# Kernel optimization log

Hardware: AMD Instinct MI355X
Metric: run time of the kernel (lower is better)

## Reference

```python
import jax, jax.numpy as jnp
import numpy as np

DIM = 1024
NUM_HEADS = 8
HEAD_DIM = 64
QK_DIM = NUM_HEADS * HEAD_DIM  # 512
B, S = 4, 1024


def setup_inputs() -> dict:
    key = jax.random.key(0)
    k1, k2, k3, k4, k5 = jax.random.split(key, 5)
    x = jax.random.normal(k1, (B, S, DIM), dtype=jnp.float32)
    mask = jax.random.randint(k2, (B, S), 0, 2).astype(bool)
    rotator = jax.random.normal(k3, (B, S, HEAD_DIM, HEAD_DIM), dtype=jnp.float32)
    # Linear weights stored as [in, out] for x @ W
    w_t = jax.random.normal(k4, (DIM, 2 * QK_DIM + DIM), dtype=jnp.float32) * (DIM ** -0.5)
    w_o = jax.random.normal(k5, (DIM, DIM), dtype=jnp.float32) * (DIM ** -0.5)
    return {"x": x, "mask": mask, "rotator": rotator, "w_t": w_t, "w_o": w_o}


def taylor_atn_fn(qs, ks, vs, mask):
    # 2nd-order Taylor approximation of softmax attention:
    # exp(s) ~= 1 + s + s^2/2, with invalid keys masked out.
    scale = HEAD_DIM ** -0.5
    s = jnp.einsum('bqhd,bkhd->bhqk', qs, ks) * scale  # [B,H,S,S]
    scores = 1.0 + s + 0.5 * s * s
    scores = scores * mask[:, None, None, :].astype(scores.dtype)  # mask keys
    denom = jnp.maximum(jnp.sum(scores, axis=-1), 1e-6)            # [B,H,Q]
    out = jnp.einsum('bhqk,bkhd->bqhd', scores, vs)
    out = out / jnp.transpose(denom, (0, 2, 1))[..., None]         # [B,Q,H,vd]
    return out.reshape(out.shape[0], out.shape[1], -1)


def reference(x, mask, rotator, w_t, w_o):
    t = x @ w_t                                   # [B,S,2*QK+DIM]
    Bx, Sx = t.shape[0], t.shape[1]
    qs = t[..., :QK_DIM].reshape(Bx, Sx, NUM_HEADS, HEAD_DIM)
    ks = t[..., QK_DIM:2 * QK_DIM].reshape(Bx, Sx, NUM_HEADS, HEAD_DIM)
    vs = t[..., 2 * QK_DIM:].reshape(Bx, Sx, NUM_HEADS, -1)
    m = mask[..., None, None]
    # masked per-position rotation: q -> R q, k -> R^T k
    qs = jnp.where(m, jnp.einsum('bsij,bshj->bshi', rotator, qs), qs)
    ks = jnp.where(m, jnp.einsum('bsij,bshi->bshj', rotator, ks), ks)
    out = taylor_atn_fn(qs, ks, vs, mask)
    return out @ w_o
```

## Files before the change

kernel.cpp:

```cpp
#include <hip/hip_runtime.h>
#include <cstdint>
#include <cstddef>

#define DIMX  1024
#define NH    8
#define HD    64
#define QKD   512
#define VDD   128
#define BATCH 4
#define SEQ   1024
#define NPOS  (BATCH*SEQ)
#define TW    (2*QKD + DIMX)
#define SCALE 0.125f

typedef __bf16 bf16x8 __attribute__((ext_vector_type(8)));
typedef float  f32x4  __attribute__((ext_vector_type(4)));
typedef float  f32x16 __attribute__((ext_vector_type(16)));

__device__ __forceinline__ ushort f2bf(float f) {
    unsigned b = __float_as_uint(f);
    return (ushort)((b + 0x7FFFu + ((b >> 16) & 1u)) >> 16);
}

__device__ __forceinline__ unsigned cvtpk(float lo, float hi) {
    unsigned r;
    asm("v_cvt_pk_bf16_f32 %0, %1, %2" : "=v"(r) : "v"(lo), "v"(hi));
    return r;
}

__device__ __forceinline__ void plswap(unsigned &a, unsigned &b) {
    asm("v_permlane32_swap_b32 %0, %1" : "+v"(a), "+v"(b));
}

#define GLD16(src, dst) __builtin_amdgcn_global_load_lds(                      \
    (const __attribute__((address_space(1))) unsigned int*)(src),              \
    (__attribute__((address_space(3))) unsigned int*)(dst), 16, 0, 0)

#define SW(row, col) ((row)*64 + ((col) ^ (((row)&7)<<3)))

__device__ __forceinline__ int2 xcd_swz(int gx, int gy) {
    const int nwg = gx * gy;
    int id = blockIdx.y * gx + blockIdx.x;
    id = (id & 7) * (nwg >> 3) + (id >> 3);
    return make_int2(id % gx, id / gx);
}

__global__ __launch_bounds__(256)
void cast_bf16(const float* __restrict__ in, ushort* __restrict__ out, int n4)
{
    const int i = blockIdx.x * 256 + threadIdx.x;
    if (i >= n4) return;
    float4 v = *(const float4*)(in + (size_t)i * 4);
    ushort4 o;
    o.x = f2bf(v.x); o.y = f2bf(v.y); o.z = f2bf(v.z); o.w = f2bf(v.w);
    *(ushort4*)(out + (size_t)i * 4) = o;
}

__global__ __launch_bounds__(256)
void transpose_cast(const float* __restrict__ W, ushort* __restrict__ WT,
                    int K, int N)
{
    __shared__ float tile[32][33];
    const int bn = blockIdx.x * 32;
    const int bk = blockIdx.y * 32;
    const int tx = threadIdx.x & 31;
    const int ty = threadIdx.x >> 5;
    #pragma unroll
    for (int i = ty; i < 32; i += 8)
        tile[i][tx] = W[(size_t)(bk + i) * N + bn + tx];
    __syncthreads();
    #pragma unroll
    for (int i = ty; i < 32; i += 8)
        WT[(size_t)(bn + i) * K + bk + tx] = f2bf(tile[tx][i]);
}

__global__ __launch_bounds__(256, 2)
void gemm_qkv(const ushort* __restrict__ A, const ushort* __restrict__ BT,
              float* __restrict__ t1, ushort* __restrict__ Vt)
{
    const int K = DIMX, N = TW;
    __shared__ __align__(16) ushort lA[128 * 32];
    __shared__ __align__(16) ushort lB[128 * 32];

    const int2 bij = xcd_swz(N/128, NPOS/128);
    const int tid  = threadIdx.x;
    const int lane = tid & 63;
    const int wave = tid >> 6;
    const int wr   = wave >> 1;
    const int wc   = wave & 1;
    const int bm   = bij.y * 128;
    const int bn   = bij.x * 128;

    const int r0 = wave * 32 + (lane >> 2);
    const int kc = (lane & 3) * 8;
    const ushort* a0 = A  + (size_t)(bm + r0) * K + kc;
    const ushort* a1 = A  + (size_t)(bm + r0 + 16) * K + kc;
    const ushort* b0 = BT + (size_t)(bn + r0) * K + kc;
    const ushort* b1 = BT + (size_t)(bn + r0 + 16) * K + kc;
    ushort* lA0 = lA + wave * 1024;
    ushort* lA1 = lA0 + 512;
    ushort* lB0 = lB + wave * 1024;
    ushort* lB1 = lB0 + 512;

    const int fr = lane & 15;
    const int kh = (lane >> 4) * 8;
    const ushort* ra = lA + (wr * 64 + fr) * 32 + kh;
    const ushort* rb = lB + (wc * 64 + fr) * 32 + kh;

    f32x4 acc[4][4] = {};

    for (int k0 = 0; k0 < K; k0 += 32) {
        GLD16(a0 + k0, lA0);
        GLD16(a1 + k0, lA1);
        GLD16(b0 + k0, lB0);
        GLD16(b1 + k0, lB1);
        asm volatile("s_waitcnt vmcnt(0)" ::: "memory");
        __syncthreads();
        bf16x8 af[4], bfr[4];
        #pragma unroll
        for (int m = 0; m < 4; ++m) af[m]  = *(const bf16x8*)(ra + m * 512);
        #pragma unroll
        for (int n = 0; n < 4; ++n) bfr[n] = *(const bf16x8*)(rb + n * 512);
        #pragma unroll
        for (int m = 0; m < 4; ++m)
            #pragma unroll
            for (int n = 0; n < 4; ++n)
                acc[m][n] = __builtin_amdgcn_mfma_f32_16x16x32_bf16(
                    af[m], bfr[n], acc[m][n], 0, 0, 0);
        __syncthreads();
    }

    const int orow = (lane >> 4) * 4;
    if (bn < 1024) {
        #pragma unroll
        for (int m = 0; m < 4; ++m)
            #pragma unroll
            for (int n = 0; n < 4; ++n) {
                float* dst = t1 + (size_t)(bm + wr * 64 + m * 16 + orow) * 1024
                               + bn + wc * 64 + n * 16 + fr;
                #pragma unroll
                for (int q = 0; q < 4; ++q)
                    dst[(size_t)q * 1024] = acc[m][n][q];
            }
    } else {
        #pragma unroll
        for (int m = 0; m < 4; ++m)
            #pragma unroll
            for (int n = 0; n < 4; ++n) {
                const int row0 = bm + wr * 64 + m * 16 + orow;
                const int cv   = bn + wc * 64 + n * 16 + fr - 1024;
                const int hh = cv >> 7, vd = cv & 127;
                const int bb = row0 >> 10, ss = row0 & 1023;
                ushort o4[4];
                #pragma unroll
                for (int q = 0; q < 4; ++q) o4[q] = f2bf(acc[m][n][q]);
                *(ushort4*)&Vt[((size_t)(bb*NH + hh)*VDD + vd)*SEQ + ss] =
                    *(ushort4*)o4;
            }
    }
}

__global__ __launch_bounds__(256, 2)
void gemm_bf16_mfma(const ushort* __restrict__ A, const ushort* __restrict__ BT,
                    float* __restrict__ C, int M, int N, int K)
{
    __shared__ __align__(16) ushort lA[128 * 32];
    __shared__ __align__(16) ushort lB[128 * 32];

    const int2 bij = xcd_swz(N/128, M/128);
    const int tid  = threadIdx.x;
    const int lane = tid & 63;
    const int wave = tid >> 6;
    const int wr   = wave >> 1;
    const int wc   = wave & 1;
    const int bm   = bij.y * 128;
    const int bn   = bij.x * 128;

    const int r0 = wave * 32 + (lane >> 2);
    const int kc = (lane & 3) * 8;
    const ushort* a0 = A  + (size_t)(bm + r0) * K + kc;
    const ushort* a1 = A  + (size_t)(bm + r0 + 16) * K + kc;
    const ushort* b0 = BT + (size_t)(bn + r0) * K + kc;
    const ushort* b1 = BT + (size_t)(bn + r0 + 16) * K + kc;
    ushort* lA0 = lA + wave * 1024;
    ushort* lA1 = lA0 + 512;
    ushort* lB0 = lB + wave * 1024;
    ushort* lB1 = lB0 + 512;

    const int fr = lane & 15;
    const int kh = (lane >> 4) * 8;
    const ushort* ra = lA + (wr * 64 + fr) * 32 + kh;
    const ushort* rb = lB + (wc * 64 + fr) * 32 + kh;

    f32x4 acc[4][4] = {};

    for (int k0 = 0; k0 < K; k0 += 32) {
        GLD16(a0 + k0, lA0);
        GLD16(a1 + k0, lA1);
        GLD16(b0 + k0, lB0);
        GLD16(b1 + k0, lB1);
        asm volatile("s_waitcnt vmcnt(0)" ::: "memory");
        __syncthreads();
        bf16x8 af[4], bfr[4];
        #pragma unroll
        for (int m = 0; m < 4; ++m) af[m]  = *(const bf16x8*)(ra + m * 512);
        #pragma unroll
        for (int n = 0; n < 4; ++n) bfr[n] = *(const bf16x8*)(rb + n * 512);
        #pragma unroll
        for (int m = 0; m < 4; ++m)
            #pragma unroll
            for (int n = 0; n < 4; ++n)
                acc[m][n] = __builtin_amdgcn_mfma_f32_16x16x32_bf16(
                    af[m], bfr[n], acc[m][n], 0, 0, 0);
        __syncthreads();
    }

    const int orow = (lane >> 4) * 4;
    #pragma unroll
    for (int m = 0; m < 4; ++m)
        #pragma unroll
        for (int n = 0; n < 4; ++n) {
            float* dst = C + (size_t)(bm + wr * 64 + m * 16 + orow) * N
                           + bn + wc * 64 + n * 16 + fr;
            #pragma unroll
            for (int q = 0; q < 4; ++q)
                dst[(size_t)q * N] = acc[m][n][q];
        }
}

__global__ __launch_bounds__(256)
void rotate_pack_qk(const float* __restrict__ t1, const int* __restrict__ mask,
                    const float* __restrict__ rot, ushort* __restrict__ Qb,
                    ushort* __restrict__ Kb)
{
    const int p   = blockIdx.x;
    const int tid = threadIdx.x;
    const int b = p >> 10, s = p & 1023;
    const bool rotated = (mask[p] != 0);

    __shared__ float R[64][69];
    __shared__ float qv[QKD];
    __shared__ float kv[QKD];

    const float* tq = t1 + (size_t)p * 1024;
    {
        float2 q2 = *(const float2*)(tq + tid*2);
        float2 k2 = *(const float2*)(tq + QKD + tid*2);
        qv[tid*2]   = q2.x; qv[tid*2+1] = q2.y;
        kv[tid*2]   = k2.x; kv[tid*2+1] = k2.y;
        if (rotated) {
            const float* Rg = rot + (size_t)p * 4096;
            const int base = tid * 16;
            const int r = base >> 6, c = base & 63;
            #pragma unroll
            for (int x = 0; x < 16; x += 4) {
                float4 v = *(const float4*)(Rg + base + x);
                R[r][c+x+0] = v.x; R[r][c+x+1] = v.y;
                R[r][c+x+2] = v.z; R[r][c+x+3] = v.w;
            }
        }
    }
    __syncthreads();

    #pragma unroll
    for (int ph = 0; ph < 2; ++ph) {
        const int h = (tid >> 6) + ph*4;
        const int i = tid & 63;
        const float* qh  = &qv[h*64];
        const float* kh2 = &kv[h*64];
        float aq, ak;
        if (rotated) {
            aq = 0.f; ak = 0.f;
            #pragma unroll 8
            for (int j = 0; j < 64; ++j) {
                aq = fmaf(R[i][j], qh[j], aq);
                ak = fmaf(R[j][i], kh2[j], ak);
            }
        } else {
            aq = qh[i]; ak = kh2[i];
        }
        const size_t dst = ((size_t)(b*NH + h)*SEQ + s)*HD + i;
        Qb[dst] = f2bf(aq * SCALE);
        Kb[dst] = f2bf(ak);
    }
}

__global__ __launch_bounds__(256, 2)
void taylor_attn_mfma(const ushort* __restrict__ Qb, const ushort* __restrict__ Kb,
                      const ushort* __restrict__ Vt, const int* __restrict__ mask,
                      ushort* __restrict__ attn)
{
    const int bh  = blockIdx.x;
    const int qt  = blockIdx.y;
    const int b   = bh >> 3, h = bh & 7;
    const int tid = threadIdx.x;
    const int lane = tid & 63;
    const int wave = tid >> 6;
    const int kh  = wave >> 1;
    const int qg  = wave & 1;
    const int l31 = lane & 31;
    const int g   = lane >> 5;

    __shared__ __align__(16) ushort smem[32768];
    __shared__ float mskAll[SEQ];
    __shared__ float dpart[64];
    __shared__ float dinv2[64];

    ushort* Ksp = smem + kh * 8192;
    ushort* Vsp = smem + 16384 + kh * 8192;
    float*  comb = (float*)smem;

    {
        int4 mv = *(const int4*)(mask + b*SEQ + tid*4);
        float4 f = make_float4(mv.x ? 1.f : 0.f, mv.y ? 1.f : 0.f,
                               mv.z ? 1.f : 0.f, mv.w ? 1.f : 0.f);
        *(float4*)&mskAll[tid*4] = f;
    }

    const ushort* qrow = Qb + ((size_t)bh*SEQ + qt*64 + qg*32 + l31) * HD + g*8;
    bf16x8 qf[4];
    #pragma unroll
    for (int ds = 0; ds < 4; ++ds) qf[ds] = *(const bf16x8*)(qrow + ds*16);

    const int sub  = lane >> 3;
    const int scol = ((lane & 7) * 8) ^ (sub << 3);
    const ushort* Kbase = Kb + (size_t)bh*SEQ*HD;
    const ushort* Vbase = Vt + (size_t)bh*VDD*SEQ;

#define ISSUE_K(buf, ktn) do {                                                 \
    _Pragma("unroll")                                                          \
    for (int i_ = 0; i_ < 4; ++i_)                                             \
        GLD16(Kbase + ((size_t)(ktn)*64 + 8*(qg*4+i_) + sub)*HD + scol,        \
              Ksp + (buf)*4096 + (qg*4+i_)*512);                               \
} while (0)
#define ISSUE_V(ktn) do {                                                      \
    _Pragma("unroll")                                                          \
    for (int i_ = 0; i_ < 8; ++i_)                                             \
        GLD16(Vbase + (size_t)(8*(qg*8+i_) + sub)*SEQ + (ktn)*64 + scol,       \
              Vsp + (qg*8+i_)*512);                                            \
} while (0)

    f32x16 acc[4] = {};
    float dacc = 0.f;

    ISSUE_K(0, kh*8);
    asm volatile("s_waitcnt vmcnt(0)" ::: "memory");
    __syncthreads();

    for (int it = 0; it < 8; ++it) {
        const int kt = kh*8 + it;
        const int cb = it & 1;
        ISSUE_V(kt);
        if (it < 7) ISSUE_K(cb ^ 1, kt + 1);

        f32x16 sf0 = {}, sf1 = {};
        __builtin_amdgcn_s_setprio(1);
        #pragma unroll
        for (int ds = 0; ds < 4; ++ds) {
            const int dc = ds*16 + g*8;
            bf16x8 kf0 = *(const bf16x8*)&Ksp[cb*4096 + SW(l31, dc)];
            bf16x8 kf1 = *(const bf16x8*)&Ksp[cb*4096 + SW(32 + l31, dc)];
            sf0 = __builtin_amdgcn_mfma_f32_32x32x16_bf16(kf0, qf[ds], sf0, 0, 0, 0);
            sf1 = __builtin_amdgcn_mfma_f32_32x32x16_bf16(kf1, qf[ds], sf1, 0, 0, 0);
        }
        __builtin_amdgcn_s_setprio(0);

        const float* mrow = mskAll + kt*64;
        unsigned w0[8], w1[8];
        float dadd = 0.f;
        #pragma unroll
        for (int rr = 0; rr < 4; ++rr) {
            const float4 mqa = *(const float4*)&mrow[8*rr + 4*g];
            const float4 mqb = *(const float4*)&mrow[32 + 8*rr + 4*g];
            float s0 = sf0[rr*4+0], s1 = sf0[rr*4+1];
            float s2 = sf0[rr*4+2], s3 = sf0[rr*4+3];
            float c0 = fmaf(fmaf(0.5f*s0, s0, s0), mqa.x, mqa.x);
            float c1 = fmaf(fmaf(0.5f*s1, s1, s1), mqa.y, mqa.y);
            float c2 = fmaf(fmaf(0.5f*s2, s2, s2), mqa.z, mqa.z);
            float c3 = fmaf(fmaf(0.5f*s3, s3, s3), mqa.w, mqa.w);
            float t0 = sf1[rr*4+0], t1 = sf1[rr*4+1];
            float t2 = sf1[rr*4+2], t3 = sf1[rr*4+3];
            float d0 = fmaf(fmaf(0.5f*t0, t0, t0), mqb.x, mqb.x);
            float d1 = fmaf(fmaf(0.5f*t1, t1, t1), mqb.y, mqb.y);
            float d2 = fmaf(fmaf(0.5f*t2, t2, t2), mqb.z, mqb.z);
            float d3 = fmaf(fmaf(0.5f*t3, t3, t3), mqb.w, mqb.w);
            dadd += ((c0+c1)+(c2+c3)) + ((d0+d1)+(d2+d3));
            w0[rr*2+0] = cvtpk(c0, c1);
            w0[rr*2+1] = cvtpk(c2, c3);
            w1[rr*2+0] = cvtpk(d0, d1);
            w1[rr*2+1] = cvtpk(d2, d3);
        }
        dacc += dadd;
        plswap(w0[0], w0[2]); plswap(w0[1], w0[3]);
        plswap(w0[4], w0[6]); plswap(w0[5], w0[7]);
        plswap(w1[0], w1[2]); plswap(w1[1], w1[3]);
        plswap(w1[4], w1[6]); plswap(w1[5], w1[7]);

        asm volatile("s_waitcnt vmcnt(0)" ::: "memory");
        __syncthreads();

        __builtin_amdgcn_s_setprio(1);
        #pragma unroll
        for (int kq = 0; kq < 4; ++kq) {
            union { unsigned u[4]; bf16x8 v; } pu;
            if (kq == 0)      { pu.u[0]=w0[0]; pu.u[1]=w0[1]; pu.u[2]=w0[2]; pu.u[3]=w0[3]; }
            else if (kq == 1) { pu.u[0]=w0[4]; pu.u[1]=w0[5]; pu.u[2]=w0[6]; pu.u[3]=w0[7]; }
            else if (kq == 2) { pu.u[0]=w1[0]; pu.u[1]=w1[1]; pu.u[2]=w1[2]; pu.u[3]=w1[3]; }
            else              { pu.u[0]=w1[4]; pu.u[1]=w1[5]; pu.u[2]=w1[6]; pu.u[3]=w1[7]; }
            const int kcol = kq*16 + g*8;
            acc[0] = __builtin_amdgcn_mfma_f32_32x32x16_bf16(
                pu.v, *(const bf16x8*)&Vsp[SW(      l31, kcol)], acc[0], 0, 0, 0);
            acc[1] = __builtin_amdgcn_mfma_f32_32x32x16_bf16(
                pu.v, *(const bf16x8*)&Vsp[SW( 32 + l31, kcol)], acc[1], 0, 0, 0);
            acc[2] = __builtin_amdgcn_mfma_f32_32x32x16_bf16(
                pu.v, *(const bf16x8*)&Vsp[SW( 64 + l31, kcol)], acc[2], 0, 0, 0);
            acc[3] = __builtin_amdgcn_mfma_f32_32x32x16_bf16(
                pu.v, *(const bf16x8*)&Vsp[SW( 96 + l31, kcol)], acc[3], 0, 0, 0);
        }
        __builtin_amdgcn_s_setprio(0);
        __syncthreads();
    }
#undef ISSUE_K
#undef ISSUE_V

    const float dhalf = dacc + __shfl_xor(dacc, 32);

    if (kh == 1) {
        float* cbp = comb + qg * 4096;
        #pragma unroll
        for (int vb = 0; vb < 4; ++vb)
            #pragma unroll
            for (int rr = 0; rr < 4; ++rr) {
                float4 v = make_float4(acc[vb][rr*4+0], acc[vb][rr*4+1],
                                       acc[vb][rr*4+2], acc[vb][rr*4+3]);
                *(float4*)&cbp[(vb*32 + l31)*32 + 4*g + 8*rr] = v;
            }
        if (lane < 32) dpart[qg*32 + l31] = dhalf;
    }
    __syncthreads();
    if (kh == 0) {
        float* cbp = comb + qg * 4096;
        const float dtot = dhalf + dpart[qg*32 + l31];
        if (lane < 32) dinv2[qg*32 + l31] = 1.f / fmaxf(dtot, 1e-6f);
        #pragma unroll
        for (int vb = 0; vb < 4; ++vb)
            #pragma unroll
            for (int rr = 0; rr < 4; ++rr) {
                float4 v = *(const float4*)&cbp[(vb*32 + l31)*32 + 4*g + 8*rr];
                acc[vb][rr*4+0] += v.x; acc[vb][rr*4+1] += v.y;
                acc[vb][rr*4+2] += v.z; acc[vb][rr*4+3] += v.w;
            }
        float inv[16];
        #pragma unroll
        for (int rr = 0; rr < 4; ++rr) {
            float4 iv = *(const float4*)&dinv2[qg*32 + 8*rr + 4*g];
            inv[rr*4+0] = iv.x; inv[rr*4+1] = iv.y;
            inv[rr*4+2] = iv.z; inv[rr*4+3] = iv.w;
        }
        ushort* obase = attn + ((size_t)(b*SEQ + qt*64 + qg*32)) * DIMX
                      + h*VDD + l31;
        #pragma unroll
        for (int vb = 0; vb < 4; ++vb)
            #pragma unroll
            for (int rr = 0; rr < 4; ++rr)
                #pragma unroll
                for (int j = 0; j < 4; ++j) {
                    const int q = 4*g + 8*rr + j;
                    obase[(size_t)q*DIMX + vb*32] = f2bf(acc[vb][rr*4+j] * inv[rr*4+j]);
                }
    }
}

extern "C" void kernel_launch(void* const* d_in, const int* in_sizes, int n_in,
                              void* d_out, int out_size, void* d_ws, size_t ws_size,
                              hipStream_t stream)
{
    const float* x    = (const float*)d_in[0];
    const int*   mask = (const int*)d_in[1];
    const float* rot  = (const float*)d_in[2];
    const float* w_t  = (const float*)d_in[3];
    const float* w_o  = (const float*)d_in[4];
    float* out = (float*)d_out;

    float*  t1     = (float*)d_ws;
    ushort* xbf    = (ushort*)(t1 + (size_t)NPOS * 1024);
    ushort* attnbf = xbf;
    ushort* wtT    = xbf + (size_t)NPOS * DIMX;
    ushort* woT    = wtT + (size_t)TW * DIMX;
    ushort* Qb     = woT + (size_t)DIMX * DIMX;
    ushort* Kb     = Qb  + (size_t)BATCH * NH * SEQ * HD;
    ushort* Vtp    = Kb  + (size_t)BATCH * NH * SEQ * HD;

    cast_bf16<<<(NPOS*DIMX/4 + 255)/256, 256, 0, stream>>>(x, xbf, NPOS*DIMX/4);
    transpose_cast<<<dim3(TW/32, DIMX/32),   256, 0, stream>>>(w_t, wtT, DIMX, TW);
    transpose_cast<<<dim3(DIMX/32, DIMX/32), 256, 0, stream>>>(w_o, woT, DIMX, DIMX);

    gemm_qkv<<<dim3(TW/128, NPOS/128), 256, 0, stream>>>(xbf, wtT, t1, Vtp);
    rotate_pack_qk<<<NPOS, 256, 0, stream>>>(t1, mask, rot, Qb, Kb);
    taylor_attn_mfma<<<dim3(BATCH*NH, SEQ/64), 256, 0, stream>>>(Qb, Kb, Vtp, mask, attnbf);
    gemm_bf16_mfma<<<dim3(DIMX/128, NPOS/128), 256, 0, stream>>>(attnbf, woT, out, NPOS, DIMX, DIMX);
}
```

Baseline: 110.8 us.

## Store QK projection as bf16 and use partial vmcnt waits in attention

The QKV GEMM now writes the Q/K projection intermediate as bf16 instead of fp32, and the rotate kernel reads bf16 and widens it to float. This halves the traffic of that intermediate buffer in both kernels, at the cost of rounding Q/K to bf16 before the rotation. The attention loop also swaps full vmcnt(0) waits plus __syncthreads for counted vmcnt waits and raw s_barrier. The next K tile's loads can then stay in flight while the current tile is computed, but correctness now depends on the exact count of outstanding loads.

```diff
diff --git a/kernel.cpp b/kernel.cpp
--- a/kernel.cpp
+++ b/kernel.cpp
@@ -20,6 +20,9 @@
 __device__ __forceinline__ ushort f2bf(float f) {
     unsigned b = __float_as_uint(f);
     return (ushort)((b + 0x7FFFu + ((b >> 16) & 1u)) >> 16);
+}
+__device__ __forceinline__ float bf2f(ushort u) {
+    return __uint_as_float((unsigned)u << 16);
 }
 
 __device__ __forceinline__ unsigned cvtpk(float lo, float hi) {
@@ -76,7 +79,7 @@
 
 __global__ __launch_bounds__(256, 2)
 void gemm_qkv(const ushort* __restrict__ A, const ushort* __restrict__ BT,
-              float* __restrict__ t1, ushort* __restrict__ Vt)
+              ushort* __restrict__ t1b, ushort* __restrict__ Vt)
 {
     const int K = DIMX, N = TW;
     __shared__ __align__(16) ushort lA[128 * 32];
@@ -136,11 +139,11 @@
         for (int m = 0; m < 4; ++m)
             #pragma unroll
             for (int n = 0; n < 4; ++n) {
-                float* dst = t1 + (size_t)(bm + wr * 64 + m * 16 + orow) * 1024
-                               + bn + wc * 64 + n * 16 + fr;
+                ushort* dst = t1b + (size_t)(bm + wr * 64 + m * 16 + orow) * 1024
+                                  + bn + wc * 64 + n * 16 + fr;
                 #pragma unroll
                 for (int q = 0; q < 4; ++q)
-                    dst[(size_t)q * 1024] = acc[m][n][q];
+                    dst[(size_t)q * 1024] = f2bf(acc[m][n][q]);
             }
     } else {
         #pragma unroll
@@ -229,7 +232,7 @@
 }
 
 __global__ __launch_bounds__(256)
-void rotate_pack_qk(const float* __restrict__ t1, const int* __restrict__ mask,
+void rotate_pack_qk(const ushort* __restrict__ t1b, const int* __restrict__ mask,
                     const float* __restrict__ rot, ushort* __restrict__ Qb,
                     ushort* __restrict__ Kb)
 {
@@ -242,12 +245,12 @@
     __shared__ float qv[QKD];
     __shared__ float kv[QKD];
 
-    const float* tq = t1 + (size_t)p * 1024;
+    const ushort* tq = t1b + (size_t)p * 1024;
     {
-        float2 q2 = *(const float2*)(tq + tid*2);
-        float2 k2 = *(const float2*)(tq + QKD + tid*2);
-        qv[tid*2]   = q2.x; qv[tid*2+1] = q2.y;
-        kv[tid*2]   = k2.x; kv[tid*2+1] = k2.y;
+        ushort2 q2 = *(const ushort2*)(tq + tid*2);
+        ushort2 k2 = *(const ushort2*)(tq + QKD + tid*2);
+        qv[tid*2]   = bf2f(q2.x); qv[tid*2+1] = bf2f(q2.y);
+        kv[tid*2]   = bf2f(k2.x); kv[tid*2+1] = bf2f(k2.y);
         if (rotated) {
             const float* Rg = rot + (size_t)p * 4096;
             const int base = tid * 16;
@@ -343,15 +346,20 @@
     f32x16 acc[4] = {};
     float dacc = 0.f;
 
+    __syncthreads();
     ISSUE_K(0, kh*8);
-    asm volatile("s_waitcnt vmcnt(0)" ::: "memory");
-    __syncthreads();
 
     for (int it = 0; it < 8; ++it) {
         const int kt = kh*8 + it;
         const int cb = it & 1;
         ISSUE_V(kt);
-        if (it < 7) ISSUE_K(cb ^ 1, kt + 1);
+        if (it < 7) {
+            ISSUE_K(cb ^ 1, kt + 1);
+            asm volatile("s_waitcnt vmcnt(12)" ::: "memory");
+        } else {
+            asm volatile("s_waitcnt vmcnt(8)"  ::: "memory");
+        }
+        __builtin_amdgcn_s_barrier();
 
         f32x16 sf0 = {}, sf1 = {};
         __builtin_amdgcn_s_setprio(1);
@@ -396,8 +404,9 @@
         plswap(w1[0], w1[2]); plswap(w1[1], w1[3]);
         plswap(w1[4], w1[6]); plswap(w1[5], w1[7]);
 
-        asm volatile("s_waitcnt vmcnt(0)" ::: "memory");
-        __syncthreads();
+        if (it < 7) asm volatile("s_waitcnt vmcnt(4)" ::: "memory");
+        else        asm volatile("s_waitcnt vmcnt(0)" ::: "memory");
+        __builtin_amdgcn_s_barrier();
 
         __builtin_amdgcn_s_setprio(1);
         #pragma unroll
@@ -418,7 +427,7 @@
                 pu.v, *(const bf16x8*)&Vsp[SW( 96 + l31, kcol)], acc[3], 0, 0, 0);
         }
         __builtin_amdgcn_s_setprio(0);
-        __syncthreads();
+        __builtin_amdgcn_s_barrier();
     }
 #undef ISSUE_K
 #undef ISSUE_V
@@ -482,8 +491,8 @@
     const float* w_o  = (const float*)d_in[4];
     float* out = (float*)d_out;
 
-    float*  t1     = (float*)d_ws;
-    ushort* xbf    = (ushort*)(t1 + (size_t)NPOS * 1024);
+    ushort* t1b    = (ushort*)d_ws;
+    ushort* xbf    = t1b + (size_t)NPOS * 1024;
     ushort* attnbf = xbf;
     ushort* wtT    = xbf + (size_t)NPOS * DIMX;
     ushort* woT    = wtT + (size_t)TW * DIMX;
@@ -495,8 +504,8 @@
     transpose_cast<<<dim3(TW/32, DIMX/32),   256, 0, stream>>>(w_t, wtT, DIMX, TW);
     transpose_cast<<<dim3(DIMX/32, DIMX/32), 256, 0, stream>>>(w_o, woT, DIMX, DIMX);
 
-    gemm_qkv<<<dim3(TW/128, NPOS/128), 256, 0, stream>>>(xbf, wtT, t1, Vtp);
-    rotate_pack_qk<<<NPOS, 256, 0, stream>>>(t1, mask, rot, Qb, Kb);
+    gemm_qkv<<<dim3(TW/128, NPOS/128), 256, 0, stream>>>(xbf, wtT, t1b, Vtp);
+    rotate_pack_qk<<<NPOS, 256, 0, stream>>>(t1b, mask, rot, Qb, Kb);
     taylor_attn_mfma<<<dim3(BATCH*NH, SEQ/64), 256, 0, stream>>>(Qb, Kb, Vtp, mask, attnbf);
     gemm_bf16_mfma<<<dim3(DIMX/128, NPOS/128), 256, 0, stream>>>(attnbf, woT, out, NPOS, DIMX, DIMX);
 }
```

Result: no change. 111.4 us (+0.6%).
